# Kernel tuning notes

Hardware: AMD Instinct MI355X
Metric: run time of the kernel (lower is better)

The kernel has to match this reference:

```python
import jax, jax.numpy as jnp
import numpy as np

B, Hn, Wn, C, NH, WS, SR = 4, 64, 64, 256, 8, 3, 8
HD = C // NH
N = Hn * Wn
L = WS * WS
PH, PW = Hn // SR, Wn // SR
P = PH * PW
T = 4096  # cpb table length
NEG = -1e30

def _l2norm(x, axis=-1):
    return x / jnp.maximum(jnp.linalg.norm(x, axis=axis, keepdims=True), 1e-12)

def _unfold(x, ws):
    # x: (B, C, H, W) -> (B, C, ws*ws, H*W), torch F.unfold channel ordering (C major)
    p = ws // 2
    b, c, h, w = x.shape
    xp = jnp.pad(x, ((0, 0), (0, 0), (p, p), (p, p)))
    pats = jnp.stack([xp[:, :, i:i + h, j:j + w] for i in range(ws) for j in range(ws)], axis=2)
    return pats.reshape(b, c, ws * ws, h * w)

def setup_inputs():
    key = jax.random.key(0)
    ks = jax.random.split(key, 16)
    def w(k, shape, s=0.02):
        return jax.random.normal(k, shape, jnp.float32) * s
    # buffers derived from the window geometry (get_seqlen_and_mask)
    ones = np.ones((Hn, Wn), np.float32)
    pad = WS // 2
    op = np.pad(ones, pad)
    pats = np.stack([op[i:i + Hn, j:j + Wn] for i in range(WS) for j in range(WS)], -1).reshape(N, L)
    padding_mask = jnp.asarray(pats == 0)
    seq_length_scale = jnp.asarray(np.log(pats.sum(-1, keepdims=True) + P).astype(np.float32))
    temperature = jnp.log(jnp.expm1(jnp.ones((NH, 1, 1), jnp.float32) / 0.24))
    return dict(
        x=jax.random.normal(ks[0], (B, N, C), jnp.float32),
        relative_pos_index=jax.random.randint(ks[1], (N, P), 0, T),
        relative_coords_table=jax.random.uniform(ks[2], (T, 2), jnp.float32, -1.0, 1.0),
        q_w=w(ks[3], (C, C)), q_b=jnp.zeros((C,), jnp.float32),
        kv_w=w(ks[4], (2 * C, C)), kv_b=jnp.zeros((2 * C,), jnp.float32),
        temperature=temperature,
        query_embedding=w(ks[5], (NH, 1, HD)),
        proj_w=w(ks[6], (C, C)), proj_b=jnp.zeros((C,), jnp.float32),
        sr_w=w(ks[7], (C, C)), sr_b=jnp.zeros((C,), jnp.float32),
        norm_g=jnp.ones((C,), jnp.float32), norm_b=jnp.zeros((C,), jnp.float32),
        cpb1_w=w(ks[8], (512, 2)), cpb1_b=jnp.zeros((512,), jnp.float32),
        cpb2_w=w(ks[9], (NH, 512)), cpb2_b=jnp.zeros((NH,), jnp.float32),
        rpb_local=w(ks[10], (NH, L), 0.0004),
        learnable_tokens=w(ks[11], (NH, HD, L)),
        learnable_bias=jnp.zeros((NH, 1, L), jnp.float32),
        seq_length_scale=seq_length_scale,
        padding_mask=padding_mask,
        H=Hn, W=Wn,
    )

def _forward(x, q_w, q_b, kv_w, kv_b, temperature, query_embedding, proj_w, proj_b,
             sr_w, sr_b, norm_g, norm_b, cpb1_w, cpb1_b, cpb2_w, cpb2_b, rpb_local,
             learnable_tokens, learnable_bias, seq_length_scale, relative_coords_table,
             relative_pos_index, padding_mask, H, W):
    b, n, c = x.shape
    # normalized queries, scaled by learnable temperature and log-seqlen
    q = (x @ q_w.T + q_b).reshape(b, n, NH, HD).transpose(0, 2, 1, 3)  # (B,h,N,d)
    q_norm = _l2norm(q)
    q_scaled = (q_norm + query_embedding[None]) * jax.nn.softplus(temperature)[None] * seq_length_scale
    # --- local branch: sliding-window QK with RPB ---
    kv = x @ kv_w.T + kv_b  # (B,N,2C)
    k_loc = _l2norm((kv[..., :c]).reshape(b, n, NH, HD)).reshape(b, n, c)
    kv_img = jnp.concatenate([k_loc, kv[..., c:]], -1).transpose(0, 2, 1).reshape(b, 2 * c, H, W)
    pats = _unfold(kv_img, WS).reshape(b, 2 * NH, HD, L, n).transpose(0, 1, 4, 2, 3)  # (B,2h,N,d,L)
    k_loc, v_loc = pats[:, :NH], pats[:, NH:]
    attn_local = jnp.einsum('bhnd,bhndl->bhnl', q_scaled, k_loc) + rpb_local[None, :, None, :]
    attn_local = jnp.where(padding_mask[None, None], NEG, attn_local)
    # --- pooled branch ---
    x_img = x.transpose(0, 2, 1).reshape(b, c, H, W)
    x_sr = jax.nn.gelu(jnp.einsum('bchw,oc->bohw', x_img, sr_w) + sr_b[None, :, None, None], approximate=False)
    x_pool = x_sr.reshape(b, c, PH, SR, PW, SR).mean((3, 5)).reshape(b, c, P).transpose(0, 2, 1)  # (B,P,C)
    mu = x_pool.mean(-1, keepdims=True)
    var = x_pool.var(-1, keepdims=True)
    x_pool = (x_pool - mu) / jnp.sqrt(var + 1e-5) * norm_g + norm_b
    kv_pool = (x_pool @ kv_w.T + kv_b).reshape(b, P, 2 * NH, HD).transpose(0, 2, 1, 3)
    k_pool, v_pool = kv_pool[:, :NH], kv_pool[:, NH:]  # (B,h,P,d)
    cpb = jax.nn.relu(relative_coords_table @ cpb1_w.T + cpb1_b) @ cpb2_w.T + cpb2_b  # (T,h)
    pool_bias = cpb.T[:, relative_pos_index.reshape(-1)].reshape(NH, n, P)
    attn_pool = jnp.einsum('bhnd,bhpd->bhnp', q_scaled, _l2norm(k_pool)) + pool_bias[None]
    # --- joint softmax over local + pooled keys ---
    attn = jax.nn.softmax(jnp.concatenate([attn_local, attn_pool], -1), axis=-1)
    attn_local, attn_pool = attn[..., :L], attn[..., L:]
    a = jnp.einsum('bhnd,hdl->bhnl', q_norm, learnable_tokens) + learnable_bias[None] + attn_local
    x_local = jnp.einsum('bhnl,bhndl->bhnd', a, v_loc)
    x_pool_out = jnp.einsum('bhnp,bhpd->bhnd', attn_pool, v_pool)
    out = (x_local + x_pool_out).transpose(0, 2, 1, 3).reshape(b, n, c)
    return out @ proj_w.T + proj_b

def reference(x, relative_pos_index, relative_coords_table, q_w, q_b, kv_w, kv_b, temperature,
              query_embedding, proj_w, proj_b, sr_w, sr_b, norm_g, norm_b, cpb1_w, cpb1_b,
              cpb2_w, cpb2_b, rpb_local, learnable_tokens, learnable_bias, seq_length_scale,
              padding_mask, H, W):
    return _forward(x, q_w, q_b, kv_w, kv_b, temperature, query_embedding, proj_w, proj_b,
                    sr_w, sr_b, norm_g, norm_b, cpb1_w, cpb1_b, cpb2_w, cpb2_b, rpb_local,
                    learnable_tokens, learnable_bias, seq_length_scale, relative_coords_table,
                    relative_pos_index, padding_mask, H, W)
```

## Files before the change

kernel.cpp:

```cpp
#include <hip/hip_runtime.h>
#include <hip/hip_bf16.h>

typedef unsigned short u16;
typedef unsigned int u32;

#define B_ 4
#define N_ 4096
#define C_ 256
#define NH_ 8
#define HD_ 32
#define L_ 9
#define P_ 64
#define T_ 4096
#define NEG_ (-1e30f)

typedef __attribute__((ext_vector_type(8))) short bf16x8;
typedef __attribute__((ext_vector_type(4))) float f32x4;

__device__ __forceinline__ float b2f(u16 u) {
    union { u32 i; float f; } v; v.i = ((u32)u) << 16; return v.f;
}
__device__ __forceinline__ u16 f2b(float f) {
    u32 x = __float_as_uint(f);
    u32 r = (x + 0x7fffu + ((x >> 16) & 1u)) >> 16;
    return (u16)r;
}
__device__ __forceinline__ short f2bs(float f) { return (short)f2b(f); }

__global__ __launch_bounds__(256) void prep_k(
    const float* __restrict__ x, const float* __restrict__ q_w, const float* __restrict__ kv_w,
    const float* __restrict__ sr_w, const float* __restrict__ proj_w,
    u16* __restrict__ xb, u16* __restrict__ wfused, u16* __restrict__ pwb,
    const float* __restrict__ table, const float* __restrict__ w1, const float* __restrict__ b1,
    const float* __restrict__ w2, const float* __restrict__ b2, float* __restrict__ cpb)
{
    __shared__ float w1s[512][2];
    __shared__ float b1s[512];
    __shared__ float w2s[8][512];
    int bid = blockIdx.x, tid = threadIdx.x;
    if (bid < 4096) {
        int i = bid * 256 + tid;
        float4 v = reinterpret_cast<const float4*>(x)[i];
        ushort4 o; o.x = f2b(v.x); o.y = f2b(v.y); o.z = f2b(v.z); o.w = f2b(v.w);
        reinterpret_cast<ushort4*>(xb)[i] = o;
    } else if (bid < 4416) {
        int i = (bid - 4096) * 256 + tid;
        const float* s; u16* d; int off;
        if (i < 16384)      { s = q_w;    d = wfused; off = i; }
        else if (i < 49152) { s = kv_w;   d = wfused; off = i; }
        else if (i < 65536) { s = sr_w;   d = wfused; off = i; }
        else                { s = proj_w; d = pwb;    off = i - 65536; }
        int soff = (i < 16384) ? i : (i < 49152) ? (i - 16384) : (i < 65536) ? (i - 49152) : (i - 65536);
        float4 v = reinterpret_cast<const float4*>(s)[soff];
        ushort4 o; o.x = f2b(v.x); o.y = f2b(v.y); o.z = f2b(v.z); o.w = f2b(v.w);
        reinterpret_cast<ushort4*>(d)[off] = o;
    } else {
        for (int i = tid; i < 512; i += 256) {
            w1s[i][0] = w1[i * 2]; w1s[i][1] = w1[i * 2 + 1]; b1s[i] = b1[i];
        }
        for (int i = tid; i < 4096; i += 256) w2s[i >> 9][i & 511] = w2[i];
        __syncthreads();
        int t = (bid - 4416) * 256 + tid;
        float t0 = table[t * 2], t1 = table[t * 2 + 1];
        float acc[8] = {};
        for (int j = 0; j < 512; ++j) {
            float h = fmaxf(t0 * w1s[j][0] + t1 * w1s[j][1] + b1s[j], 0.0f);
            #pragma unroll
            for (int hh = 0; hh < 8; ++hh) acc[hh] += h * w2s[hh][j];
        }
        #pragma unroll
        for (int hh = 0; hh < 8; ++hh) cpb[t * 8 + hh] = acc[hh] + b2[hh];
    }
}

template<int MODE>
__global__ __launch_bounds__(256) void gemm_big_k(
    const u16* __restrict__ A, const u16* __restrict__ W,
    const float* __restrict__ b0, const float* __restrict__ b1, const float* __restrict__ b2,
    float* __restrict__ kvk, u16* __restrict__ kvv, u16* __restrict__ xgb, float* __restrict__ pout)
{
    constexpr int RI = (MODE == 0) ? 4 : 2;
    __shared__ u16 Bs[64 * 264];
    int tid = threadIdx.x, w = tid >> 6, lane = tid & 63;
    int quad = lane >> 4, l16 = lane & 15;
    int colBase = (MODE == 0 ? 256 : 0) + blockIdx.x * 64;
    #pragma unroll
    for (int c = 0; c < 8; ++c) {
        int linear = c * 256 + tid;
        int col = linear >> 5, kc = linear & 31;
        uint4 v = *reinterpret_cast<const uint4*>(W + (size_t)(colBase + col) * 256 + kc * 8);
        *reinterpret_cast<uint4*>(&Bs[col * 264 + kc * 8]) = v;
    }
    __syncthreads();
    int rowBase = blockIdx.y * (RI * 64) + w * (RI * 16);
    f32x4 acc[RI][4] = {};
    const u16* aptr = A + (size_t)(rowBase + l16) * 256 + quad * 8;
    bf16x8 afc[RI];
    #pragma unroll
    for (int i = 0; i < RI; ++i) afc[i] = *reinterpret_cast<const bf16x8*>(aptr + (size_t)i * 16 * 256);
    #pragma unroll
    for (int k0 = 0; k0 < 256; k0 += 32) {
        bf16x8 afn[RI];
        if (k0 < 224) {
            #pragma unroll
            for (int i = 0; i < RI; ++i)
                afn[i] = *reinterpret_cast<const bf16x8*>(aptr + (size_t)i * 16 * 256 + k0 + 32);
        }
        #pragma unroll
        for (int j = 0; j < 4; ++j) {
            bf16x8 bfr = *reinterpret_cast<const bf16x8*>(&Bs[(j * 16 + l16) * 264 + k0 + quad * 8]);
            #pragma unroll
            for (int i = 0; i < RI; ++i)
                acc[i][j] = __builtin_amdgcn_mfma_f32_16x16x32_bf16(afc[i], bfr, acc[i][j], 0, 0, 0);
        }
        if (k0 < 224) {
            #pragma unroll
            for (int i = 0; i < RI; ++i) afc[i] = afn[i];
        }
    }
    int rng = (MODE == 0) ? (colBase >> 8) : 99;
    float bj[4];
    #pragma unroll
    for (int j = 0; j < 4; ++j) {
        int gc = colBase + j * 16 + l16;
        if (MODE == 1)      bj[j] = b0[gc];
        else if (rng <= 2)  bj[j] = b1[gc - 256];
        else                bj[j] = b2[gc - 768];
    }
    #pragma unroll
    for (int i = 0; i < RI; ++i) {
        float vals[4][4];
        #pragma unroll
        for (int j = 0; j < 4; ++j)
            #pragma unroll
            for (int r = 0; r < 4; ++r) {
                float t = acc[i][j][r] + bj[j];
                if (MODE == 0 && rng == 3) t = 0.5f * t * (1.0f + erff(t * 0.70710678118654752f));
                vals[j][r] = t;
            }
        if (MODE == 0 && rng == 1) {
            #pragma unroll
            for (int hp = 0; hp < 2; ++hp)
                #pragma unroll
                for (int r = 0; r < 4; ++r) {
                    float s = vals[2*hp][r] * vals[2*hp][r] + vals[2*hp+1][r] * vals[2*hp+1][r];
                    s += __shfl_xor(s, 1); s += __shfl_xor(s, 2);
                    s += __shfl_xor(s, 4); s += __shfl_xor(s, 8);
                    float inv = 1.0f / fmaxf(sqrtf(s), 1e-12f);
                    vals[2*hp][r] *= inv; vals[2*hp+1][r] *= inv;
                }
        }
        #pragma unroll
        for (int j = 0; j < 4; ++j) {
            int gc = colBase + j * 16 + l16;
            #pragma unroll
            for (int r = 0; r < 4; ++r) {
                int row = rowBase + i * 16 + quad * 4 + r;
                if (MODE == 1)      pout[(size_t)row * 256 + gc] = vals[j][r];
                else if (rng == 1)  kvk[(size_t)row * 256 + gc - 256] = vals[j][r];
                else if (rng == 2)  kvv[(size_t)row * 256 + gc - 512] = f2b(vals[j][r]);
                else                xgb[(size_t)row * 256 + gc - 768] = f2b(vals[j][r]);
            }
        }
    }
}

__global__ __launch_bounds__(256) void poolkv_k(
    const u16* __restrict__ xgb, const float* __restrict__ g, const float* __restrict__ bta,
    const float* __restrict__ kv_w, const float* __restrict__ kv_b, float* __restrict__ kvp,
    const int* __restrict__ rpi, const float* __restrict__ cpb, float* __restrict__ biasp)
{
    int bid = blockIdx.x;
    int tid = threadIdx.x;
    if (bid >= 512) {
        int i = (bid - 512) * 256 + tid;
        int e0 = i * 4;
        int p = e0 & 63;
        int hn = e0 >> 6;
        int n = hn & 4095, h = hn >> 12;
        int4 idx4 = *reinterpret_cast<const int4*>(rpi + n * 64 + p);
        float4 o;
        o.x = cpb[(size_t)idx4.x * 8 + h];
        o.y = cpb[(size_t)idx4.y * 8 + h];
        o.z = cpb[(size_t)idx4.z * 8 + h];
        o.w = cpb[(size_t)idx4.w * 8 + h];
        *reinterpret_cast<float4*>(biasp + e0) = o;
        return;
    }
    __shared__ __align__(16) float xps[256];
    __shared__ float r1[4], r2[4];
    int bp = bid >> 1, half = bid & 1;
    int b = bp >> 6, p = bp & 63;
    int py = p >> 3, px = p & 7;
    int o = tid;
    float s = 0.0f;
    for (int sy = 0; sy < 8; ++sy)
        #pragma unroll
        for (int sx = 0; sx < 8; ++sx) {
            int pix = (py * 8 + sy) * 64 + px * 8 + sx;
            s += b2f(xgb[((size_t)(b * N_ + pix)) * C_ + o]);
        }
    float v = s * (1.0f / 64.0f);
    float s1 = v, s2 = v * v;
    #pragma unroll
    for (int off = 32; off >= 1; off >>= 1) { s1 += __shfl_xor(s1, off); s2 += __shfl_xor(s2, off); }
    int wv = o >> 6, ln = o & 63;
    if (ln == 0) { r1[wv] = s1; r2[wv] = s2; }
    __syncthreads();
    float S1 = r1[0] + r1[1] + r1[2] + r1[3];
    float S2 = r2[0] + r2[1] + r2[2] + r2[3];
    float mu = S1 * (1.0f / 256.0f);
    float var = S2 * (1.0f / 256.0f) - mu * mu;
    xps[o] = (v - mu) * rsqrtf(var + 1e-5f) * g[o] + bta[o];
    __syncthreads();
    int col = half * 256 + o;
    float a = kv_b[col];
    const float4* xp4 = (const float4*)xps;
    const float4* wrow = (const float4*)(kv_w + (size_t)col * 256);
    #pragma unroll 8
    for (int k4 = 0; k4 < 64; ++k4) {
        float4 xv = xp4[k4]; float4 wa = wrow[k4];
        a += xv.x * wa.x + xv.y * wa.y + xv.z * wa.z + xv.w * wa.w;
    }
    if (half == 0) {
        float ss = a * a;
        ss += __shfl_xor(ss, 1); ss += __shfl_xor(ss, 2); ss += __shfl_xor(ss, 4);
        ss += __shfl_xor(ss, 8); ss += __shfl_xor(ss, 16);
        a *= 1.0f / fmaxf(sqrtf(ss), 1e-12f);
    }
    kvp[(size_t)bp * 512 + col] = a;
}

__global__ __launch_bounds__(256) void attn_k(
    const u16* __restrict__ xb, const u16* __restrict__ qwb, const float* __restrict__ q_b,
    const float* __restrict__ kvk, const u16* __restrict__ kvv,
    const float* __restrict__ kvp, const float* __restrict__ biasp,
    const float* __restrict__ temp, const float* __restrict__ qe, const float* __restrict__ lt,
    const float* __restrict__ rpb, const float* __restrict__ lb,
    const float* __restrict__ slsin, u16* __restrict__ aob)
{
    __shared__ u16 kp_hi[64 * 40], kp_lo[64 * 40];
    __shared__ u16 vp_hi[32 * 72], vp_lo[32 * 72];
    __shared__ u16 ltb[16 * 32];
    __shared__ float S_w[4][16][76];
    __shared__ float qs_l[4][16][36];
    __shared__ float rpb_s[9], lb_s[9];

    int bid = blockIdx.x;
    int tile = bid & 63, h = (bid >> 6) & 7, b = bid >> 9;
    int tid = threadIdx.x, wave = tid >> 6, lane = tid & 63;
    int quad = lane >> 4, l16 = lane & 15;

    {
        int p = tid >> 2, dc = (tid & 3) * 8;
        const float* src = kvp + ((size_t)(b * P_ + p)) * 512 + h * 32 + dc;
        float4 k0 = *(const float4*)(src), k1 = *(const float4*)(src + 4);
        float4 v0 = *(const float4*)(src + 256), v1 = *(const float4*)(src + 260);
        float kf[8] = {k0.x,k0.y,k0.z,k0.w,k1.x,k1.y,k1.z,k1.w};
        float vf[8] = {v0.x,v0.y,v0.z,v0.w,v1.x,v1.y,v1.z,v1.w};
        #pragma unroll
        for (int j = 0; j < 8; ++j) {
            u16 khi = f2b(kf[j]);
            kp_hi[p * 40 + dc + j] = khi;
            kp_lo[p * 40 + dc + j] = f2b(kf[j] - b2f(khi));
            u16 vhi = f2b(vf[j]);
            vp_hi[(dc + j) * 72 + p] = vhi;
            vp_lo[(dc + j) * 72 + p] = f2b(vf[j] - b2f(vhi));
        }
    }
    for (int t = tid; t < 512; t += 256) {
        int l = t & 15, d = t >> 4;
        ltb[l * 32 + d] = (l < 9) ? f2b(lt[h * 288 + d * 9 + l]) : (u16)0;
    }
    if (tid < 9) { rpb_s[tid] = rpb[h * 9 + tid]; lb_s[tid] = lb[h * 9 + tid]; }
    float tsc = log1pf(expf(temp[h]));
    __syncthreads();

    int n0w = tile * 64 + wave * 16;

    f32x4 qacc[2] = {};
    {
        const u16* xrow = xb + ((size_t)(b * N_ + n0w + l16)) * 256 + quad * 8;
        const u16* qwr  = qwb + ((size_t)(h * 32 + l16)) * 256 + quad * 8;
        #pragma unroll
        for (int k0 = 0; k0 < 256; k0 += 32) {
            bf16x8 ax = *(const bf16x8*)(xrow + k0);
            bf16x8 bw0 = *(const bf16x8*)(qwr + k0);
            bf16x8 bw1 = *(const bf16x8*)(qwr + 16 * 256 + k0);
            qacc[0] = __builtin_amdgcn_mfma_f32_16x16x32_bf16(ax, bw0, qacc[0], 0, 0, 0);
            qacc[1] = __builtin_amdgcn_mfma_f32_16x16x32_bf16(ax, bw1, qacc[1], 0, 0, 0);
        }
    }
    {
        float qb0 = q_b[h * 32 + l16], qb1 = q_b[h * 32 + 16 + l16];
        float qe0 = qe[h * 32 + l16],  qe1 = qe[h * 32 + 16 + l16];
        #pragma unroll
        for (int r = 0; r < 4; ++r) {
            int p = quad * 4 + r;
            float v0 = qacc[0][r] + qb0, v1 = qacc[1][r] + qb1;
            float s = v0 * v0 + v1 * v1;
            s += __shfl_xor(s, 1); s += __shfl_xor(s, 2);
            s += __shfl_xor(s, 4); s += __shfl_xor(s, 8);
            float inv = 1.0f / fmaxf(sqrtf(s), 1e-12f);
            v0 *= inv; v1 *= inv;
            float sc = tsc * slsin[n0w + p];
            qs_l[wave][p][l16]      = (v0 + qe0) * sc;
            qs_l[wave][p][16 + l16] = (v1 + qe1) * sc;
        }
        if (quad == 0) { S_w[wave][l16][73] = NEG_; S_w[wave][l16][74] = NEG_; S_w[wave][l16][75] = NEG_; }
    }
    bf16x8 qs_hi, qs_lo, qn_b;
    float qsr[8];
    {
        *(float4*)&qsr[0] = *(const float4*)&qs_l[wave][l16][quad * 8];
        *(float4*)&qsr[4] = *(const float4*)&qs_l[wave][l16][quad * 8 + 4];
        float invs = 1.0f / (tsc * slsin[n0w + l16]);
        const float* qep = qe + h * 32 + quad * 8;
        float4 e0 = *(const float4*)qep, e1 = *(const float4*)(qep + 4);
        float ef[8] = {e0.x,e0.y,e0.z,e0.w,e1.x,e1.y,e1.z,e1.w};
        #pragma unroll
        for (int j = 0; j < 8; ++j) {
            u16 hi = f2b(qsr[j]);
            qs_hi[j] = (short)hi;
            qs_lo[j] = f2bs(qsr[j] - b2f(hi));
            qn_b[j]  = f2bs(qsr[j] * invs - ef[j]);
        }
    }
    const float* bp = biasp + (size_t)h * N_ * 64;
    #pragma unroll
    for (int jt = 0; jt < 4; ++jt) {
        bf16x8 bh = *(const bf16x8*)&kp_hi[(jt * 16 + l16) * 40 + quad * 8];
        bf16x8 bl = *(const bf16x8*)&kp_lo[(jt * 16 + l16) * 40 + quad * 8];
        f32x4 a = {};
        a = __builtin_amdgcn_mfma_f32_16x16x32_bf16(qs_lo, bh, a, 0, 0, 0);
        a = __builtin_amdgcn_mfma_f32_16x16x32_bf16(qs_hi, bl, a, 0, 0, 0);
        a = __builtin_amdgcn_mfma_f32_16x16x32_bf16(qs_hi, bh, a, 0, 0, 0);
        #pragma unroll
        for (int r = 0; r < 4; ++r) {
            int pix = quad * 4 + r;
            int n = n0w + pix;
            S_w[wave][pix][jt * 16 + l16] = a[r] + bp[(size_t)n * 64 + jt * 16 + l16];
        }
    }
    f32x4 accL;
    {
        bf16x8 ltf = *(const bf16x8*)&ltb[l16 * 32 + quad * 8];
        f32x4 z = {};
        accL = __builtin_amdgcn_mfma_f32_16x16x32_bf16(qn_b, ltf, z, 0, 0, 0);
    }
    #pragma unroll
    for (int l = 0; l < 9; ++l) {
        int n = n0w + l16, y = n >> 6, x = n & 63;
        int ny = y + l / 3 - 1, nx = x + (l % 3) - 1;
        bool ok = ((unsigned)ny < 64u) && ((unsigned)nx < 64u);
        int nn = ok ? ny * 64 + nx : n;
        const float4* kb = (const float4*)(kvk + ((size_t)(b * N_ + nn)) * 256 + h * 32 + quad * 8);
        float4 k0v = kb[0], k1v = kb[1];
        float part = qsr[0]*k0v.x + qsr[1]*k0v.y + qsr[2]*k0v.z + qsr[3]*k0v.w
                   + qsr[4]*k1v.x + qsr[5]*k1v.y + qsr[6]*k1v.z + qsr[7]*k1v.w;
        part += __shfl_xor(part, 16);
        part += __shfl_xor(part, 32);
        if (quad == 0) S_w[wave][l16][64 + l] = ok ? (part + rpb_s[l]) : NEG_;
    }
    {
        int pix = lane >> 2, c0 = (lane & 3) * 19;
        float vals[19]; float mx = NEG_;
        #pragma unroll
        for (int i = 0; i < 19; ++i) { vals[i] = S_w[wave][pix][c0 + i]; mx = fmaxf(mx, vals[i]); }
        mx = fmaxf(mx, __shfl_xor(mx, 1));
        mx = fmaxf(mx, __shfl_xor(mx, 2));
        float sm = 0.0f;
        #pragma unroll
        for (int i = 0; i < 19; ++i) { vals[i] = expf(vals[i] - mx); sm += vals[i]; }
        sm += __shfl_xor(sm, 1); sm += __shfl_xor(sm, 2);
        float inv = 1.0f / sm;
        #pragma unroll
        for (int i = 0; i < 19; ++i) S_w[wave][pix][c0 + i] = vals[i] * inv;
    }
    if (l16 < 9) {
        #pragma unroll
        for (int r = 0; r < 4; ++r) {
            int pix = quad * 4 + r;
            int n = n0w + pix, y = n >> 6, x = n & 63;
            int ny = y + l16 / 3 - 1, nx = x + (l16 % 3) - 1;
            bool ok = ((unsigned)ny < 64u) && ((unsigned)nx < 64u);
            float prev = S_w[wave][pix][64 + l16];
            S_w[wave][pix][64 + l16] = ok ? (accL[r] + lb_s[l16] + prev) : 0.0f;
        }
    }
    f32x4 accO[2] = {};
    #pragma unroll
    for (int kc = 0; kc < 2; ++kc) {
        float wf[8];
        *(float4*)&wf[0] = *(const float4*)&S_w[wave][l16][kc * 32 + quad * 8];
        *(float4*)&wf[4] = *(const float4*)&S_w[wave][l16][kc * 32 + quad * 8 + 4];
        bf16x8 w_hi, w_lo;
        #pragma unroll
        for (int j = 0; j < 8; ++j) {
            u16 hi = f2b(wf[j]);
            w_hi[j] = (short)hi;
            w_lo[j] = f2bs(wf[j] - b2f(hi));
        }
        #pragma unroll
        for (int nt = 0; nt < 2; ++nt) {
            bf16x8 vh = *(const bf16x8*)&vp_hi[(nt * 16 + l16) * 72 + kc * 32 + quad * 8];
            bf16x8 vl = *(const bf16x8*)&vp_lo[(nt * 16 + l16) * 72 + kc * 32 + quad * 8];
            accO[nt] = __builtin_amdgcn_mfma_f32_16x16x32_bf16(w_lo, vh, accO[nt], 0, 0, 0);
            accO[nt] = __builtin_amdgcn_mfma_f32_16x16x32_bf16(w_hi, vl, accO[nt], 0, 0, 0);
            accO[nt] = __builtin_amdgcn_mfma_f32_16x16x32_bf16(w_hi, vh, accO[nt], 0, 0, 0);
        }
    }
    #pragma unroll
    for (int r = 0; r < 4; ++r) {
        int pix = quad * 4 + r;
        int n = n0w + pix, y = n >> 6, x = n & 63;
        #pragma unroll
        for (int l = 0; l < 9; ++l) {
            int ny = y + l / 3 - 1, nx = x + (l % 3) - 1;
            bool ok = ((unsigned)ny < 64u) && ((unsigned)nx < 64u);
            int nn = ok ? ny * 64 + nx : n;
            float aw = S_w[wave][pix][64 + l];
            const u16* vb = kvv + ((size_t)(b * N_ + nn)) * 256 + h * 32;
            accO[0][r] += aw * b2f(vb[l16]);
            accO[1][r] += aw * b2f(vb[16 + l16]);
        }
    }
    #pragma unroll
    for (int nt = 0; nt < 2; ++nt)
        #pragma unroll
        for (int r = 0; r < 4; ++r) {
            int n = n0w + quad * 4 + r;
            aob[((size_t)(b * N_ + n)) * C_ + h * 32 + nt * 16 + l16] = f2b(accO[nt][r]);
        }
}

extern "C" void kernel_launch(void* const* d_in, const int* in_sizes, int n_in,
                              void* d_out, int out_size, void* d_ws, size_t ws_size,
                              hipStream_t stream) {
    const float* x      = (const float*)d_in[0];
    const int*   rpi    = (const int*)d_in[1];
    const float* table  = (const float*)d_in[2];
    const float* q_w    = (const float*)d_in[3];
    const float* q_b    = (const float*)d_in[4];
    const float* kv_w   = (const float*)d_in[5];
    const float* kv_b   = (const float*)d_in[6];
    const float* temp   = (const float*)d_in[7];
    const float* qe     = (const float*)d_in[8];
    const float* proj_w = (const float*)d_in[9];
    const float* proj_b = (const float*)d_in[10];
    const float* sr_w   = (const float*)d_in[11];
    const float* sr_b   = (const float*)d_in[12];
    const float* norm_g = (const float*)d_in[13];
    const float* norm_b = (const float*)d_in[14];
    const float* cpb1_w = (const float*)d_in[15];
    const float* cpb1_b = (const float*)d_in[16];
    const float* cpb2_w = (const float*)d_in[17];
    const float* cpb2_b = (const float*)d_in[18];
    const float* rpb    = (const float*)d_in[19];
    const float* lt     = (const float*)d_in[20];
    const float* lb     = (const float*)d_in[21];
    const float* sls    = (const float*)d_in[22];

    float* ws   = (float*)d_ws;
    float* kvk  = ws;
    float* kvp  = kvk + (size_t)B_ * N_ * C_;
    float* cpb  = kvp + (size_t)B_ * P_ * 2 * C_;
    float* bia  = cpb + (size_t)T_ * NH_;
    u16*   xb   = (u16*)(bia + (size_t)NH_ * N_ * P_);
    u16*   wfb  = xb  + (size_t)B_ * N_ * C_;
    u16*   pwb  = wfb + (size_t)1024 * C_;
    u16*   kvv  = pwb + (size_t)C_ * C_;
    u16*   xgb  = kvv + (size_t)B_ * N_ * C_;
    u16*   aob  = xgb;

    dim3 blk(256);

    prep_k<<<dim3(4432), blk, 0, stream>>>(x, q_w, kv_w, sr_w, proj_w, xb, wfb, pwb,
                                           table, cpb1_w, cpb1_b, cpb2_w, cpb2_b, cpb);
    gemm_big_k<0><<<dim3(12, 64), blk, 0, stream>>>(xb, wfb, nullptr, kv_b, sr_b, kvk, kvv, xgb, nullptr);
    poolkv_k<<<dim3(2560), blk, 0, stream>>>(xgb, norm_g, norm_b, kv_w, kv_b, kvp, rpi, cpb, bia);
    attn_k<<<dim3(B_ * NH_ * 64), blk, 0, stream>>>(xb, wfb, q_b, kvk, kvv, kvp, bia,
                                                    temp, qe, lt, rpb, lb, sls, aob);
    gemm_big_k<1><<<dim3(4, 128), blk, 0, stream>>>(aob, pwb, proj_b, nullptr, nullptr,
                                                    nullptr, nullptr, nullptr, (float*)d_out);
}
```

Before: 266.3 us.

## Process two tiles per attention block, drop V-lo split, reuse local V loads

Each attention block now handles two row tiles, so the pooled K/V staging into shared memory is amortised over twice as many pixels and the grid is halved. The pooled V low-part correction is removed, cutting one MFMA per step and a shared buffer, at some precision cost. The local-window V accumulation loads each neighbour once per 6-column strip and reuses it across the four pixels of a quad, instead of issuing nine loads per pixel. The projection GEMM uses one row tile per wave with a doubled grid, increasing parallelism.

```diff
diff --git a/kernel.cpp b/kernel.cpp
--- a/kernel.cpp
+++ b/kernel.cpp
@@ -79,7 +79,7 @@
     const float* __restrict__ b0, const float* __restrict__ b1, const float* __restrict__ b2,
     float* __restrict__ kvk, u16* __restrict__ kvv, u16* __restrict__ xgb, float* __restrict__ pout)
 {
-    constexpr int RI = (MODE == 0) ? 4 : 2;
+    constexpr int RI = (MODE == 0) ? 4 : 1;
     __shared__ u16 Bs[64 * 264];
     int tid = threadIdx.x, w = tid >> 6, lane = tid & 63;
     int quad = lane >> 4, l16 = lane & 15;
@@ -240,14 +240,14 @@
     const float* __restrict__ slsin, u16* __restrict__ aob)
 {
     __shared__ u16 kp_hi[64 * 40], kp_lo[64 * 40];
-    __shared__ u16 vp_hi[32 * 72], vp_lo[32 * 72];
+    __shared__ u16 vp_hi[32 * 72];
     __shared__ u16 ltb[16 * 32];
     __shared__ float S_w[4][16][76];
     __shared__ float qs_l[4][16][36];
     __shared__ float rpb_s[9], lb_s[9];
 
     int bid = blockIdx.x;
-    int tile = bid & 63, h = (bid >> 6) & 7, b = bid >> 9;
+    int tq = bid & 31, h = (bid >> 5) & 7, b = bid >> 8;
     int tid = threadIdx.x, wave = tid >> 6, lane = tid & 63;
     int quad = lane >> 4, l16 = lane & 15;
 
@@ -263,9 +263,7 @@
             u16 khi = f2b(kf[j]);
             kp_hi[p * 40 + dc + j] = khi;
             kp_lo[p * 40 + dc + j] = f2b(kf[j] - b2f(khi));
-            u16 vhi = f2b(vf[j]);
-            vp_hi[(dc + j) * 72 + p] = vhi;
-            vp_lo[(dc + j) * 72 + p] = f2b(vf[j] - b2f(vhi));
+            vp_hi[(dc + j) * 72 + p] = f2b(vf[j]);
         }
     }
     for (int t = tid; t < 512; t += 256) {
@@ -276,162 +274,177 @@
     float tsc = log1pf(expf(temp[h]));
     __syncthreads();
 
-    int n0w = tile * 64 + wave * 16;
-
-    f32x4 qacc[2] = {};
-    {
-        const u16* xrow = xb + ((size_t)(b * N_ + n0w + l16)) * 256 + quad * 8;
-        const u16* qwr  = qwb + ((size_t)(h * 32 + l16)) * 256 + quad * 8;
-        #pragma unroll
-        for (int k0 = 0; k0 < 256; k0 += 32) {
-            bf16x8 ax = *(const bf16x8*)(xrow + k0);
-            bf16x8 bw0 = *(const bf16x8*)(qwr + k0);
-            bf16x8 bw1 = *(const bf16x8*)(qwr + 16 * 256 + k0);
-            qacc[0] = __builtin_amdgcn_mfma_f32_16x16x32_bf16(ax, bw0, qacc[0], 0, 0, 0);
-            qacc[1] = __builtin_amdgcn_mfma_f32_16x16x32_bf16(ax, bw1, qacc[1], 0, 0, 0);
-        }
-    }
-    {
-        float qb0 = q_b[h * 32 + l16], qb1 = q_b[h * 32 + 16 + l16];
-        float qe0 = qe[h * 32 + l16],  qe1 = qe[h * 32 + 16 + l16];
-        #pragma unroll
-        for (int r = 0; r < 4; ++r) {
-            int p = quad * 4 + r;
-            float v0 = qacc[0][r] + qb0, v1 = qacc[1][r] + qb1;
-            float s = v0 * v0 + v1 * v1;
-            s += __shfl_xor(s, 1); s += __shfl_xor(s, 2);
-            s += __shfl_xor(s, 4); s += __shfl_xor(s, 8);
-            float inv = 1.0f / fmaxf(sqrtf(s), 1e-12f);
-            v0 *= inv; v1 *= inv;
-            float sc = tsc * slsin[n0w + p];
-            qs_l[wave][p][l16]      = (v0 + qe0) * sc;
-            qs_l[wave][p][16 + l16] = (v1 + qe1) * sc;
-        }
-        if (quad == 0) { S_w[wave][l16][73] = NEG_; S_w[wave][l16][74] = NEG_; S_w[wave][l16][75] = NEG_; }
-    }
-    bf16x8 qs_hi, qs_lo, qn_b;
-    float qsr[8];
-    {
-        *(float4*)&qsr[0] = *(const float4*)&qs_l[wave][l16][quad * 8];
-        *(float4*)&qsr[4] = *(const float4*)&qs_l[wave][l16][quad * 8 + 4];
-        float invs = 1.0f / (tsc * slsin[n0w + l16]);
-        const float* qep = qe + h * 32 + quad * 8;
-        float4 e0 = *(const float4*)qep, e1 = *(const float4*)(qep + 4);
-        float ef[8] = {e0.x,e0.y,e0.z,e0.w,e1.x,e1.y,e1.z,e1.w};
-        #pragma unroll
-        for (int j = 0; j < 8; ++j) {
-            u16 hi = f2b(qsr[j]);
-            qs_hi[j] = (short)hi;
-            qs_lo[j] = f2bs(qsr[j] - b2f(hi));
-            qn_b[j]  = f2bs(qsr[j] * invs - ef[j]);
-        }
-    }
-    const float* bp = biasp + (size_t)h * N_ * 64;
-    #pragma unroll
-    for (int jt = 0; jt < 4; ++jt) {
-        bf16x8 bh = *(const bf16x8*)&kp_hi[(jt * 16 + l16) * 40 + quad * 8];
-        bf16x8 bl = *(const bf16x8*)&kp_lo[(jt * 16 + l16) * 40 + quad * 8];
-        f32x4 a = {};
-        a = __builtin_amdgcn_mfma_f32_16x16x32_bf16(qs_lo, bh, a, 0, 0, 0);
-        a = __builtin_amdgcn_mfma_f32_16x16x32_bf16(qs_hi, bl, a, 0, 0, 0);
-        a = __builtin_amdgcn_mfma_f32_16x16x32_bf16(qs_hi, bh, a, 0, 0, 0);
-        #pragma unroll
-        for (int r = 0; r < 4; ++r) {
-            int pix = quad * 4 + r;
-            int n = n0w + pix;
-            S_w[wave][pix][jt * 16 + l16] = a[r] + bp[(size_t)n * 64 + jt * 16 + l16];
-        }
-    }
-    f32x4 accL;
-    {
-        bf16x8 ltf = *(const bf16x8*)&ltb[l16 * 32 + quad * 8];
-        f32x4 z = {};
-        accL = __builtin_amdgcn_mfma_f32_16x16x32_bf16(qn_b, ltf, z, 0, 0, 0);
-    }
-    #pragma unroll
-    for (int l = 0; l < 9; ++l) {
-        int n = n0w + l16, y = n >> 6, x = n & 63;
-        int ny = y + l / 3 - 1, nx = x + (l % 3) - 1;
-        bool ok = ((unsigned)ny < 64u) && ((unsigned)nx < 64u);
-        int nn = ok ? ny * 64 + nx : n;
-        const float4* kb = (const float4*)(kvk + ((size_t)(b * N_ + nn)) * 256 + h * 32 + quad * 8);
-        float4 k0v = kb[0], k1v = kb[1];
-        float part = qsr[0]*k0v.x + qsr[1]*k0v.y + qsr[2]*k0v.z + qsr[3]*k0v.w
-                   + qsr[4]*k1v.x + qsr[5]*k1v.y + qsr[6]*k1v.z + qsr[7]*k1v.w;
-        part += __shfl_xor(part, 16);
-        part += __shfl_xor(part, 32);
-        if (quad == 0) S_w[wave][l16][64 + l] = ok ? (part + rpb_s[l]) : NEG_;
-    }
-    {
-        int pix = lane >> 2, c0 = (lane & 3) * 19;
-        float vals[19]; float mx = NEG_;
-        #pragma unroll
-        for (int i = 0; i < 19; ++i) { vals[i] = S_w[wave][pix][c0 + i]; mx = fmaxf(mx, vals[i]); }
-        mx = fmaxf(mx, __shfl_xor(mx, 1));
-        mx = fmaxf(mx, __shfl_xor(mx, 2));
-        float sm = 0.0f;
-        #pragma unroll
-        for (int i = 0; i < 19; ++i) { vals[i] = expf(vals[i] - mx); sm += vals[i]; }
-        sm += __shfl_xor(sm, 1); sm += __shfl_xor(sm, 2);
-        float inv = 1.0f / sm;
-        #pragma unroll
-        for (int i = 0; i < 19; ++i) S_w[wave][pix][c0 + i] = vals[i] * inv;
-    }
-    if (l16 < 9) {
-        #pragma unroll
-        for (int r = 0; r < 4; ++r) {
-            int pix = quad * 4 + r;
-            int n = n0w + pix, y = n >> 6, x = n & 63;
-            int ny = y + l16 / 3 - 1, nx = x + (l16 % 3) - 1;
-            bool ok = ((unsigned)ny < 64u) && ((unsigned)nx < 64u);
-            float prev = S_w[wave][pix][64 + l16];
-            S_w[wave][pix][64 + l16] = ok ? (accL[r] + lb_s[l16] + prev) : 0.0f;
-        }
-    }
-    f32x4 accO[2] = {};
-    #pragma unroll
-    for (int kc = 0; kc < 2; ++kc) {
-        float wf[8];
-        *(float4*)&wf[0] = *(const float4*)&S_w[wave][l16][kc * 32 + quad * 8];
-        *(float4*)&wf[4] = *(const float4*)&S_w[wave][l16][kc * 32 + quad * 8 + 4];
-        bf16x8 w_hi, w_lo;
-        #pragma unroll
-        for (int j = 0; j < 8; ++j) {
-            u16 hi = f2b(wf[j]);
-            w_hi[j] = (short)hi;
-            w_lo[j] = f2bs(wf[j] - b2f(hi));
-        }
-        #pragma unroll
-        for (int nt = 0; nt < 2; ++nt) {
-            bf16x8 vh = *(const bf16x8*)&vp_hi[(nt * 16 + l16) * 72 + kc * 32 + quad * 8];
-            bf16x8 vl = *(const bf16x8*)&vp_lo[(nt * 16 + l16) * 72 + kc * 32 + quad * 8];
-            accO[nt] = __builtin_amdgcn_mfma_f32_16x16x32_bf16(w_lo, vh, accO[nt], 0, 0, 0);
-            accO[nt] = __builtin_amdgcn_mfma_f32_16x16x32_bf16(w_hi, vl, accO[nt], 0, 0, 0);
-            accO[nt] = __builtin_amdgcn_mfma_f32_16x16x32_bf16(w_hi, vh, accO[nt], 0, 0, 0);
-        }
-    }
-    #pragma unroll
-    for (int r = 0; r < 4; ++r) {
-        int pix = quad * 4 + r;
-        int n = n0w + pix, y = n >> 6, x = n & 63;
+    const float* bp_h = biasp + (size_t)h * N_ * 64;
+
+    for (int it = 0; it < 2; ++it) {
+        int tile = tq * 2 + it;
+        int n0w = tile * 64 + wave * 16;
+        int y = tile;
+
+        f32x4 qacc[2] = {};
+        {
+            const u16* xrow = xb + ((size_t)(b * N_ + n0w + l16)) * 256 + quad * 8;
+            const u16* qwr  = qwb + ((size_t)(h * 32 + l16)) * 256 + quad * 8;
+            #pragma unroll
+            for (int k0 = 0; k0 < 256; k0 += 32) {
+                bf16x8 ax = *(const bf16x8*)(xrow + k0);
+                bf16x8 bw0 = *(const bf16x8*)(qwr + k0);
+                bf16x8 bw1 = *(const bf16x8*)(qwr + 16 * 256 + k0);
+                qacc[0] = __builtin_amdgcn_mfma_f32_16x16x32_bf16(ax, bw0, qacc[0], 0, 0, 0);
+                qacc[1] = __builtin_amdgcn_mfma_f32_16x16x32_bf16(ax, bw1, qacc[1], 0, 0, 0);
+            }
+        }
+        {
+            float qb0 = q_b[h * 32 + l16], qb1 = q_b[h * 32 + 16 + l16];
+            float qe0 = qe[h * 32 + l16],  qe1 = qe[h * 32 + 16 + l16];
+            #pragma unroll
+            for (int r = 0; r < 4; ++r) {
+                int p = quad * 4 + r;
+                float v0 = qacc[0][r] + qb0, v1 = qacc[1][r] + qb1;
+                float s = v0 * v0 + v1 * v1;
+                s += __shfl_xor(s, 1); s += __shfl_xor(s, 2);
+                s += __shfl_xor(s, 4); s += __shfl_xor(s, 8);
+                float inv = 1.0f / fmaxf(sqrtf(s), 1e-12f);
+                v0 *= inv; v1 *= inv;
+                float sc = tsc * slsin[n0w + p];
+                qs_l[wave][p][l16]      = (v0 + qe0) * sc;
+                qs_l[wave][p][16 + l16] = (v1 + qe1) * sc;
+            }
+        }
+        bf16x8 qs_hi, qs_lo, qn_b;
+        float qsr[8];
+        {
+            *(float4*)&qsr[0] = *(const float4*)&qs_l[wave][l16][quad * 8];
+            *(float4*)&qsr[4] = *(const float4*)&qs_l[wave][l16][quad * 8 + 4];
+            float invs = 1.0f / (tsc * slsin[n0w + l16]);
+            const float* qep = qe + h * 32 + quad * 8;
+            float4 e0 = *(const float4*)qep, e1 = *(const float4*)(qep + 4);
+            float ef[8] = {e0.x,e0.y,e0.z,e0.w,e1.x,e1.y,e1.z,e1.w};
+            #pragma unroll
+            for (int j = 0; j < 8; ++j) {
+                u16 hi = f2b(qsr[j]);
+                qs_hi[j] = (short)hi;
+                qs_lo[j] = f2bs(qsr[j] - b2f(hi));
+                qn_b[j]  = f2bs(qsr[j] * invs - ef[j]);
+            }
+        }
+        #pragma unroll
+        for (int jt = 0; jt < 4; ++jt) {
+            bf16x8 bh = *(const bf16x8*)&kp_hi[(jt * 16 + l16) * 40 + quad * 8];
+            bf16x8 bl = *(const bf16x8*)&kp_lo[(jt * 16 + l16) * 40 + quad * 8];
+            f32x4 a = {};
+            a = __builtin_amdgcn_mfma_f32_16x16x32_bf16(qs_lo, bh, a, 0, 0, 0);
+            a = __builtin_amdgcn_mfma_f32_16x16x32_bf16(qs_hi, bl, a, 0, 0, 0);
+            a = __builtin_amdgcn_mfma_f32_16x16x32_bf16(qs_hi, bh, a, 0, 0, 0);
+            #pragma unroll
+            for (int r = 0; r < 4; ++r) {
+                int pix = quad * 4 + r;
+                int n = n0w + pix;
+                S_w[wave][pix][jt * 16 + l16] = a[r] + bp_h[(size_t)n * 64 + jt * 16 + l16];
+            }
+        }
+        f32x4 accL;
+        {
+            bf16x8 ltf = *(const bf16x8*)&ltb[l16 * 32 + quad * 8];
+            f32x4 z = {};
+            accL = __builtin_amdgcn_mfma_f32_16x16x32_bf16(qn_b, ltf, z, 0, 0, 0);
+        }
         #pragma unroll
         for (int l = 0; l < 9; ++l) {
+            int n = n0w + l16, x = n & 63;
             int ny = y + l / 3 - 1, nx = x + (l % 3) - 1;
             bool ok = ((unsigned)ny < 64u) && ((unsigned)nx < 64u);
             int nn = ok ? ny * 64 + nx : n;
-            float aw = S_w[wave][pix][64 + l];
-            const u16* vb = kvv + ((size_t)(b * N_ + nn)) * 256 + h * 32;
-            accO[0][r] += aw * b2f(vb[l16]);
-            accO[1][r] += aw * b2f(vb[16 + l16]);
-        }
-    }
-    #pragma unroll
-    for (int nt = 0; nt < 2; ++nt)
-        #pragma unroll
-        for (int r = 0; r < 4; ++r) {
-            int n = n0w + quad * 4 + r;
-            aob[((size_t)(b * N_ + n)) * C_ + h * 32 + nt * 16 + l16] = f2b(accO[nt][r]);
-        }
+            const float4* kb = (const float4*)(kvk + ((size_t)(b * N_ + nn)) * 256 + h * 32 + quad * 8);
+            float4 k0v = kb[0], k1v = kb[1];
+            float part = qsr[0]*k0v.x + qsr[1]*k0v.y + qsr[2]*k0v.z + qsr[3]*k0v.w
+                       + qsr[4]*k1v.x + qsr[5]*k1v.y + qsr[6]*k1v.z + qsr[7]*k1v.w;
+            part += __shfl_xor(part, 16);
+            part += __shfl_xor(part, 32);
+            if (quad == 0) S_w[wave][l16][64 + l] = ok ? (part + rpb_s[l]) : NEG_;
+        }
+        if (quad == 0) { S_w[wave][l16][73] = NEG_; S_w[wave][l16][74] = NEG_; S_w[wave][l16][75] = NEG_; }
+        {
+            int pix = lane >> 2, c0 = (lane & 3) * 19;
+            float vals[19]; float mx = NEG_;
+            #pragma unroll
+            for (int i = 0; i < 19; ++i) { vals[i] = S_w[wave][pix][c0 + i]; mx = fmaxf(mx, vals[i]); }
+            mx = fmaxf(mx, __shfl_xor(mx, 1));
+            mx = fmaxf(mx, __shfl_xor(mx, 2));
+            float sm = 0.0f;
+            #pragma unroll
+            for (int i = 0; i < 19; ++i) { vals[i] = expf(vals[i] - mx); sm += vals[i]; }
+            sm += __shfl_xor(sm, 1); sm += __shfl_xor(sm, 2);
+            float inv = 1.0f / sm;
+            #pragma unroll
+            for (int i = 0; i < 19; ++i) S_w[wave][pix][c0 + i] = vals[i] * inv;
+        }
+        if (l16 < 9) {
+            #pragma unroll
+            for (int r = 0; r < 4; ++r) {
+                int pix = quad * 4 + r;
+                int n = n0w + pix, x = n & 63;
+                int ny = y + l16 / 3 - 1, nx = x + (l16 % 3) - 1;
+                bool ok = ((unsigned)ny < 64u) && ((unsigned)nx < 64u);
+                float prev = S_w[wave][pix][64 + l16];
+                S_w[wave][pix][64 + l16] = ok ? (accL[r] + lb_s[l16] + prev) : 0.0f;
+            }
+        }
+        f32x4 accO[2] = {};
+        #pragma unroll
+        for (int kc = 0; kc < 2; ++kc) {
+            float wf[8];
+            *(float4*)&wf[0] = *(const float4*)&S_w[wave][l16][kc * 32 + quad * 8];
+            *(float4*)&wf[4] = *(const float4*)&S_w[wave][l16][kc * 32 + quad * 8 + 4];
+            bf16x8 w_hi, w_lo;
+            #pragma unroll
+            for (int j = 0; j < 8; ++j) {
+                u16 hi = f2b(wf[j]);
+                w_hi[j] = (short)hi;
+                w_lo[j] = f2bs(wf[j] - b2f(hi));
+            }
+            #pragma unroll
+            for (int nt = 0; nt < 2; ++nt) {
+                bf16x8 vh = *(const bf16x8*)&vp_hi[(nt * 16 + l16) * 72 + kc * 32 + quad * 8];
+                accO[nt] = __builtin_amdgcn_mfma_f32_16x16x32_bf16(w_lo, vh, accO[nt], 0, 0, 0);
+                accO[nt] = __builtin_amdgcn_mfma_f32_16x16x32_bf16(w_hi, vh, accO[nt], 0, 0, 0);
+            }
+        }
+        {
+            int xq0 = wave * 16 + quad * 4;
+            #pragma unroll
+            for (int dy = -1; dy <= 1; ++dy) {
+                int ny = y + dy;
+                bool rowOK = ((unsigned)ny < 64u);
+                #pragma unroll
+                for (int c = 0; c < 6; ++c) {
+                    int xc = xq0 - 1 + c;
+                    bool ok = rowOK && ((unsigned)xc < 64u);
+                    int nn = ok ? ny * 64 + xc : 0;
+                    const u16* vb = kvv + ((size_t)(b * N_ + nn)) * 256 + h * 32;
+                    float v0 = b2f(vb[l16]);
+                    float v1 = b2f(vb[16 + l16]);
+                    #pragma unroll
+                    for (int r = 0; r < 4; ++r) {
+                        int dxr = c - 1 - r;
+                        if (dxr >= -1 && dxr <= 1) {
+                            int l = (dy + 1) * 3 + dxr + 1;
+                            float aw = S_w[wave][quad * 4 + r][64 + l];
+                            accO[0][r] += aw * v0;
+                            accO[1][r] += aw * v1;
+                        }
+                    }
+                }
+            }
+        }
+        #pragma unroll
+        for (int nt = 0; nt < 2; ++nt)
+            #pragma unroll
+            for (int r = 0; r < 4; ++r) {
+                int n = n0w + quad * 4 + r;
+                aob[((size_t)(b * N_ + n)) * C_ + h * 32 + nt * 16 + l16] = f2b(accO[nt][r]);
+            }
+    }
 }
 
 extern "C" void kernel_launch(void* const* d_in, const int* in_sizes, int n_in,
@@ -479,8 +492,8 @@
                                            table, cpb1_w, cpb1_b, cpb2_w, cpb2_b, cpb);
     gemm_big_k<0><<<dim3(12, 64), blk, 0, stream>>>(xb, wfb, nullptr, kv_b, sr_b, kvk, kvv, xgb, nullptr);
     poolkv_k<<<dim3(2560), blk, 0, stream>>>(xgb, norm_g, norm_b, kv_w, kv_b, kvp, rpi, cpb, bia);
-    attn_k<<<dim3(B_ * NH_ * 64), blk, 0, stream>>>(xb, wfb, q_b, kvk, kvv, kvp, bia,
+    attn_k<<<dim3(B_ * NH_ * 32), blk, 0, stream>>>(xb, wfb, q_b, kvk, kvv, kvp, bia,
                                                     temp, qe, lt, rpb, lb, sls, aob);
-    gemm_big_k<1><<<dim3(4, 128), blk, 0, stream>>>(aob, pwb, proj_b, nullptr, nullptr,
+    gemm_big_k<1><<<dim3(4, 256), blk, 0, stream>>>(aob, pwb, proj_b, nullptr, nullptr,
                                                     nullptr, nullptr, nullptr, (float*)d_out);
 }
```

After: 256.8 us. 3.6% less time.
